# Optimization experiments

Measured on AMD Instinct MI355X. Metric: run time of the kernel, lower is better.

## Reference

```python
import jax, jax.numpy as jnp
import numpy as np

N_IN = 600000
KK = 4          # kernel_size**2 offsets for 2x2 transposed conv
C_IN = 64
C_OUT = 32
N_OUT = KK * N_IN
BN_EPS = 1e-5


def setup_inputs() -> dict:
    key = jax.random.key(0)
    k1, k2 = jax.random.split(key)
    x_feats = jax.random.normal(k1, (N_IN, C_IN), dtype=jnp.float32)
    # Kaiming-ish scale for conv weights [KK, C_IN, C_OUT]
    weight = jax.random.normal(k2, (KK, C_IN, C_OUT), dtype=jnp.float32) * (1.0 / np.sqrt(C_IN * KK))
    gamma = jnp.ones((C_OUT,), dtype=jnp.float32)
    beta = jnp.zeros((C_OUT,), dtype=jnp.float32)
    # Rulebook: with stride=2/kernel=2 each input voxel i has 4 child output
    # coords; out_spatial_sparsity stores outputs in arbitrary (hash) order, so
    # permute to get irregular scatter targets. out_idx[k, i] = output row for
    # (input i, kernel offset k).
    rng = np.random.default_rng(0)
    perm = rng.permutation(N_OUT).astype(np.int32)
    out_idx = jnp.asarray(perm.reshape(N_IN, KK).T)  # [KK, N_IN]
    return {
        "x_feats": x_feats,
        "weight": weight,
        "gamma": gamma,
        "beta": beta,
        "out_idx": out_idx,
        "n_out": N_OUT,
    }


def reference(x_feats, weight, gamma, beta, out_idx, n_out):
    # Gather-GEMM-scatter sparse transposed conv:
    # per-offset GEMM: [KK, N_IN, C_OUT]
    contrib = jnp.einsum("ni,kio->kno", x_feats, weight)
    y = jnp.zeros((n_out, contrib.shape[-1]), dtype=x_feats.dtype)
    y = y.at[out_idx.reshape(-1)].add(contrib.reshape(-1, contrib.shape[-1]))
    # BatchNorm1d (training mode: batch statistics, biased var) + ReLU
    mean = jnp.mean(y, axis=0)
    var = jnp.mean(jnp.square(y - mean), axis=0)
    y_hat = (y - mean) * jax.lax.rsqrt(var + BN_EPS) * gamma + beta
    return jax.nn.relu(y_hat)
```

## Files before the change

kernel.cpp:

```cpp
#include <hip/hip_runtime.h>

#define N_IN 600000
#define KK 4
#define C_IN 64
#define C_OUT 32
#define NTOT (KK*N_IN)
#define BN_EPS 1e-5f

typedef __attribute__((ext_vector_type(8))) short short8b;
typedef __attribute__((ext_vector_type(4))) float f32x4;

#define WS_G 0
#define WS_S 4096
#define WS_SCALE 4160
#define WS_BIAS 4192
#define WS_WFRAG 4224
#define WS_PART 8320
#define PART_STRIDE 4160

__device__ __forceinline__ unsigned short f2bf(float f) {
    unsigned int u = __float_as_uint(f);
    u += 0x7fffu + ((u >> 16) & 1u);
    return (unsigned short)(u >> 16);
}

union FragU { uint4 u; short8b s; unsigned int w[4]; };

#define GPADC 68
__global__ __launch_bounds__(256) void k_gram(const float* __restrict__ x,
                                              float* __restrict__ ws, int nblk) {
    __shared__ unsigned int sm[32 * GPADC];
    const int t = threadIdx.x, wv = t >> 6, l = t & 63;
    const int il = l & 15, g = l >> 4;
    const int chunk = t & 7, r0 = t >> 3;

    FragU ones;
    ones.u = make_uint4(0x3f803f80u, 0x3f803f80u, 0x3f803f80u, 0x3f803f80u);

    f32x4 acc[4];
    f32x4 accs = (f32x4){0.f, 0.f, 0.f, 0.f};
#pragma unroll
    for (int j = 0; j < 4; ++j) acc[j] = (f32x4){0.f, 0.f, 0.f, 0.f};

    const int ntiles = N_IN / 64;
    for (int tile = blockIdx.x; tile < ntiles; tile += nblk) {
        const float* base = x + (size_t)tile * 4096;
        const float4* pa = (const float4*)(base + (2 * r0) * 64 + chunk * 8);
        const float4* pb = (const float4*)(base + (2 * r0 + 1) * 64 + chunk * 8);
        const float4 a0 = pa[0], a1 = pa[1];
        const float4 b0 = pb[0], b1 = pb[1];
        __syncthreads();
        unsigned int pk[8];
        pk[0] = (unsigned)f2bf(a0.x) | ((unsigned)f2bf(b0.x) << 16);
        pk[1] = (unsigned)f2bf(a0.y) | ((unsigned)f2bf(b0.y) << 16);
        pk[2] = (unsigned)f2bf(a0.z) | ((unsigned)f2bf(b0.z) << 16);
        pk[3] = (unsigned)f2bf(a0.w) | ((unsigned)f2bf(b0.w) << 16);
        pk[4] = (unsigned)f2bf(a1.x) | ((unsigned)f2bf(b1.x) << 16);
        pk[5] = (unsigned)f2bf(a1.y) | ((unsigned)f2bf(b1.y) << 16);
        pk[6] = (unsigned)f2bf(a1.z) | ((unsigned)f2bf(b1.z) << 16);
        pk[7] = (unsigned)f2bf(a1.w) | ((unsigned)f2bf(b1.w) << 16);
        unsigned int* dst = sm + r0 * GPADC + chunk * 8;
        *(uint4*)dst = make_uint4(pk[0], pk[1], pk[2], pk[3]);
        *(uint4*)(dst + 4) = make_uint4(pk[4], pk[5], pk[6], pk[7]);
        __syncthreads();
#pragma unroll
        for (int s = 0; s < 2; ++s) {
            short8b fr[4];
#pragma unroll
            for (int c = 0; c < 4; ++c) {
                FragU fu;
#pragma unroll
                for (int h = 0; h < 4; ++h)
                    fu.w[h] = sm[(s * 16 + g * 4 + h) * GPADC + c * 16 + il];
                fr[c] = fu.s;
            }
#pragma unroll
            for (int tj = 0; tj < 4; ++tj)
                acc[tj] = __builtin_amdgcn_mfma_f32_16x16x32_bf16(fr[wv], fr[tj], acc[tj], 0, 0, 0);
            accs = __builtin_amdgcn_mfma_f32_16x16x32_bf16(ones.s, fr[wv], accs, 0, 0, 0);
        }
    }
    float* part = ws + WS_PART + (size_t)blockIdx.x * PART_STRIDE;
#pragma unroll
    for (int tj = 0; tj < 4; ++tj)
#pragma unroll
        for (int q = 0; q < 4; ++q)
            part[(wv * 16 + g * 4 + q) * 64 + tj * 16 + il] = acc[tj][q];
    if (g == 0) part[4096 + wv * 16 + il] = accs[0];
}

__global__ __launch_bounds__(256) void k_reduce(float* __restrict__ ws, int nba) {
    const int g = blockIdx.x * 4 + (threadIdx.x >> 6);
    const int lane = threadIdx.x & 63;
    const float* p = ws + WS_PART + g;
    float s = 0.f;
    for (int b = lane; b < nba; b += 64) s += p[(size_t)b * PART_STRIDE];
#pragma unroll
    for (int m = 1; m < 64; m <<= 1) s += __shfl_xor(s, m, 64);
    if (lane == 0) ws[g] = s;
}

__global__ __launch_bounds__(256) void k_finalize(const float* __restrict__ w,
                                                  const float* __restrict__ gamma,
                                                  const float* __restrict__ beta,
                                                  float* __restrict__ ws) {
    __shared__ float Gs[4096];
    __shared__ float ssum[64];
    __shared__ float red1[256], red2[256];
    const int t = threadIdx.x;
    for (int i = t; i < 4096; i += 256) Gs[i] = ws[i];
    if (t < 64) ssum[t] = ws[WS_S + t];
    __syncthreads();
    const int sub = t >> 7;
    const int k = (t >> 5) & 3;
    const int o = t & 31;
    float wc[64];
#pragma unroll
    for (int i = 0; i < 64; ++i) wc[i] = w[(k * 64 + i) * 32 + o];
    float m1 = 0.f, m2 = 0.f;
    for (int ii = 0; ii < 32; ++ii) {
        int i = sub * 32 + ii;
        m1 = fmaf(ssum[i], wc[i], m1);
        float ti = 0.f;
#pragma unroll
        for (int j = 0; j < 64; ++j) ti = fmaf(Gs[i * 64 + j], wc[j], ti);
        m2 = fmaf(wc[i], ti, m2);
    }
    red1[t] = m1;
    red2[t] = m2;
    __syncthreads();
    if (t < 32) {
        float s1 = 0.f, s2 = 0.f;
#pragma unroll
        for (int q = 0; q < 8; ++q) {
            int idx = (q & 3) * 32 + (q >> 2) * 128 + t;
            s1 += red1[idx];
            s2 += red2[idx];
        }
        float inv = 1.f / (float)NTOT;
        float mean = s1 * inv;
        float var = s2 * inv - mean * mean;
        float rstd = rsqrtf(var + BN_EPS);
        float sc = gamma[t] * rstd;
        ws[WS_SCALE + t] = sc;
        ws[WS_BIAS + t] = beta[t] - mean * sc;
    }
}

__global__ __launch_bounds__(256) void k_prepw(const float* __restrict__ w,
                                               float* __restrict__ ws) {
    const int t = blockIdx.x * 256 + threadIdx.x;
    const int l = t & 63;
    const int s = (t >> 6) & 1;
    const int c = t >> 7;
    const int col = c * 16 + (l & 15);
    const int kk = col >> 5, o = col & 31;
    unsigned int pk[4];
#pragma unroll
    for (int jj = 0; jj < 4; ++jj) {
        const int k0 = s * 32 + ((l >> 4) << 3) + jj * 2;
        unsigned int b0 = f2bf(w[(kk * 64 + k0) * 32 + o]);
        unsigned int b1 = f2bf(w[(kk * 64 + k0 + 1) * 32 + o]);
        pk[jj] = b0 | (b1 << 16);
    }
    uint4* dst = (uint4*)(ws + WS_WFRAG);
    dst[t] = make_uint4(pk[0], pk[1], pk[2], pk[3]);
}

__global__ __launch_bounds__(256, 3) void k_main(const float* __restrict__ x,
                                                 const int* __restrict__ oidx,
                                                 const float* __restrict__ ws,
                                                 float* __restrict__ out) {
    __shared__ float ldsD[4][64 * 32];
    __shared__ int ldsO[4][64];
    const int t = threadIdx.x, wv = t >> 6, l = t & 63;
    const int il = l & 15, g = l >> 4;
    const int c8 = l & 7, g8 = l >> 3;

    const float sc0 = ws[WS_SCALE + il], sc1 = ws[WS_SCALE + 16 + il];
    const float bs0 = ws[WS_BIAS + il], bs1 = ws[WS_BIAS + 16 + il];

    const short8b* wfs = (const short8b*)(ws + WS_WFRAG);
    short8b bwf[16];
#pragma unroll
    for (int f = 0; f < 16; ++f) bwf[f] = wfs[f * 64 + l];

    float* myD = ldsD[wv];
    int* myO = ldsO[wv];

    const int wgid = blockIdx.x * 4 + wv;
    int rowbase = wgid * 80;

    float4 cur0, cur1, cur2, cur3;
    {
        const float4* ap = (const float4*)(x + (size_t)(rowbase + il) * 64 + g * 8);
        cur0 = ap[0]; cur1 = ap[1]; cur2 = ap[8]; cur3 = ap[9];
    }
    int orow_cur = oidx[g * N_IN + rowbase + il];

#pragma unroll
    for (int it = 0; it < 5; ++it) {
        myO[l] = orow_cur;

        FragU af0, af1;
        af0.w[0] = (unsigned)f2bf(cur0.x) | ((unsigned)f2bf(cur0.y) << 16);
        af0.w[1] = (unsigned)f2bf(cur0.z) | ((unsigned)f2bf(cur0.w) << 16);
        af0.w[2] = (unsigned)f2bf(cur1.x) | ((unsigned)f2bf(cur1.y) << 16);
        af0.w[3] = (unsigned)f2bf(cur1.z) | ((unsigned)f2bf(cur1.w) << 16);
        af1.w[0] = (unsigned)f2bf(cur2.x) | ((unsigned)f2bf(cur2.y) << 16);
        af1.w[1] = (unsigned)f2bf(cur2.z) | ((unsigned)f2bf(cur2.w) << 16);
        af1.w[2] = (unsigned)f2bf(cur3.x) | ((unsigned)f2bf(cur3.y) << 16);
        af1.w[3] = (unsigned)f2bf(cur3.z) | ((unsigned)f2bf(cur3.w) << 16);

        float4 nx0{}, nx1{}, nx2{}, nx3{};
        int orow_nxt = 0;
        if (it < 4) {
            const float4* ap = (const float4*)(x + (size_t)(rowbase + 16 + il) * 64 + g * 8);
            nx0 = ap[0]; nx1 = ap[1]; nx2 = ap[8]; nx3 = ap[9];
            orow_nxt = oidx[g * N_IN + rowbase + 16 + il];
        }

        f32x4 acc[8];
#pragma unroll
        for (int c = 0; c < 8; ++c) acc[c] = (f32x4){0.f, 0.f, 0.f, 0.f};
#pragma unroll
        for (int c = 0; c < 8; ++c)
            acc[c] = __builtin_amdgcn_mfma_f32_16x16x32_bf16(af0.s, bwf[c * 2 + 0], acc[c], 0, 0, 0);
#pragma unroll
        for (int c = 0; c < 8; ++c)
            acc[c] = __builtin_amdgcn_mfma_f32_16x16x32_bf16(af1.s, bwf[c * 2 + 1], acc[c], 0, 0, 0);

#pragma unroll
        for (int c = 0; c < 8; ++c) {
            const float sc = (c & 1) ? sc1 : sc0;
            const float bs = (c & 1) ? bs1 : bs0;
            const int ch = (c & 1) * 16 + il;
            const int cc = ch >> 2, wd = ch & 3;
            const int rb = (c >> 1) * 16 + g * 4;
#pragma unroll
            for (int q = 0; q < 4; ++q) {
                const int R = rb + q;
                const float v = fmaxf(0.f, fmaf(acc[c][q], sc, bs));
                myD[R * 32 + (((cc ^ (R & 7)) << 2) | wd)] = v;
            }
        }
#pragma unroll
        for (int m = 0; m < 8; ++m) {
            const int R = m * 8 + g8;
            const float4 v = *(const float4*)(myD + R * 32 + ((c8 ^ g8) << 2));
            const int orow = myO[R];
            *(float4*)(out + (size_t)orow * 32 + c8 * 4) = v;
        }

        rowbase += 16;
        cur0 = nx0; cur1 = nx1; cur2 = nx2; cur3 = nx3;
        orow_cur = orow_nxt;
    }
}

extern "C" void kernel_launch(void* const* d_in, const int* in_sizes, int n_in,
                              void* d_out, int out_size, void* d_ws, size_t ws_size,
                              hipStream_t stream) {
    const float* x = (const float*)d_in[0];
    const float* w = (const float*)d_in[1];
    const float* gamma = (const float*)d_in[2];
    const float* beta = (const float*)d_in[3];
    const int* oidx = (const int*)d_in[4];
    float* out = (float*)d_out;
    float* ws = (float*)d_ws;

    int nba = 1024;
    size_t cap = ws_size / sizeof(float);
    if (cap < (size_t)WS_PART + (size_t)nba * PART_STRIDE) {
        size_t fit = (cap - WS_PART) / PART_STRIDE;
        nba = (int)(fit < 1 ? 1 : fit);
        if (nba > 1024) nba = 1024;
    }

    hipLaunchKernelGGL(k_prepw, dim3(4), dim3(256), 0, stream, w, ws);
    hipLaunchKernelGGL(k_gram, dim3(nba), dim3(256), 0, stream, x, ws, nba);
    hipLaunchKernelGGL(k_reduce, dim3(1040), dim3(256), 0, stream, ws, nba);
    hipLaunchKernelGGL(k_finalize, dim3(1), dim3(256), 0, stream, w, gamma, beta, ws);
    hipLaunchKernelGGL(k_main, dim3(1875), dim3(256), 0, stream, x, oidx, ws, out);
}
```

Before: 231.5 us.

## Invert scatter rulebook to gather inputs and write outputs contiguously

Adds a kernel that builds the inverse of the output index map in workspace, then rewrites the main kernel to walk output rows in order. Each row gathers its source input row, runs the full 4-offset GEMM, selects the matching offset's result and writes coalesced output. This swaps random 128-byte output scatters for random input-row gathers plus an extra inverse-map scatter pass. It also computes 4x redundant MFMA work per row and drops the workspace-size fallback.

```diff
diff --git a/kernel.cpp b/kernel.cpp
--- a/kernel.cpp
+++ b/kernel.cpp
@@ -17,6 +17,8 @@
 #define WS_WFRAG 4224
 #define WS_PART 8320
 #define PART_STRIDE 4160
+#define NBA_MAX 1024
+#define WS_INV (WS_PART + NBA_MAX * PART_STRIDE)
 
 __device__ __forceinline__ unsigned short f2bf(float f) {
     unsigned int u = __float_as_uint(f);
@@ -25,6 +27,12 @@
 }
 
 union FragU { uint4 u; short8b s; unsigned int w[4]; };
+
+__global__ __launch_bounds__(256) void k_binv(const int* __restrict__ oidx,
+                                              int* __restrict__ inv) {
+    const int j = blockIdx.x * 256 + threadIdx.x;
+    if (j < NTOT) inv[oidx[j]] = j;
+}
 
 #define GPADC 68
 __global__ __launch_bounds__(256) void k_gram(const float* __restrict__ x,
@@ -167,15 +175,13 @@
     dst[t] = make_uint4(pk[0], pk[1], pk[2], pk[3]);
 }
 
-__global__ __launch_bounds__(256, 3) void k_main(const float* __restrict__ x,
-                                                 const int* __restrict__ oidx,
+__global__ __launch_bounds__(256, 3) void k_minv(const float* __restrict__ x,
+                                                 const int* __restrict__ inv,
                                                  const float* __restrict__ ws,
                                                  float* __restrict__ out) {
-    __shared__ float ldsD[4][64 * 32];
-    __shared__ int ldsO[4][64];
+    __shared__ float ldsT[4][16 * 32];
     const int t = threadIdx.x, wv = t >> 6, l = t & 63;
     const int il = l & 15, g = l >> 4;
-    const int c8 = l & 7, g8 = l >> 3;
 
     const float sc0 = ws[WS_SCALE + il], sc1 = ws[WS_SCALE + 16 + il];
     const float bs0 = ws[WS_BIAS + il], bs1 = ws[WS_BIAS + 16 + il];
@@ -185,22 +191,32 @@
 #pragma unroll
     for (int f = 0; f < 16; ++f) bwf[f] = wfs[f * 64 + l];
 
-    float* myD = ldsD[wv];
-    int* myO = ldsO[wv];
-
+    float* myT = ldsT[wv];
     const int wgid = blockIdx.x * 4 + wv;
-    int rowbase = wgid * 80;
-
+    const int base0 = wgid * 240;
+
+    int j0 = inv[base0 + il];
+    int k_cur = (j0 >= N_IN) + (j0 >= 2 * N_IN) + (j0 >= 3 * N_IN);
+    int i_cur = j0 - k_cur * N_IN;
     float4 cur0, cur1, cur2, cur3;
     {
-        const float4* ap = (const float4*)(x + (size_t)(rowbase + il) * 64 + g * 8);
+        const float4* ap = (const float4*)(x + (size_t)i_cur * 64 + g * 8);
         cur0 = ap[0]; cur1 = ap[1]; cur2 = ap[8]; cur3 = ap[9];
     }
-    int orow_cur = oidx[g * N_IN + rowbase + il];
-
-#pragma unroll
-    for (int it = 0; it < 5; ++it) {
-        myO[l] = orow_cur;
+    int j1 = inv[base0 + 16 + il];
+
+#pragma unroll 1
+    for (int it = 0; it < 15; ++it) {
+        const int base = base0 + it * 16;
+        int j2 = j1;
+        if (it < 13) j2 = inv[base + 32 + il];
+        int k_nxt = (j1 >= N_IN) + (j1 >= 2 * N_IN) + (j1 >= 3 * N_IN);
+        int i_nxt = j1 - k_nxt * N_IN;
+        float4 nx0 = cur0, nx1 = cur1, nx2 = cur2, nx3 = cur3;
+        if (it < 14) {
+            const float4* ap = (const float4*)(x + (size_t)i_nxt * 64 + g * 8);
+            nx0 = ap[0]; nx1 = ap[1]; nx2 = ap[8]; nx3 = ap[9];
+        }
 
         FragU af0, af1;
         af0.w[0] = (unsigned)f2bf(cur0.x) | ((unsigned)f2bf(cur0.y) << 16);
@@ -212,14 +228,6 @@
         af1.w[2] = (unsigned)f2bf(cur3.x) | ((unsigned)f2bf(cur3.y) << 16);
         af1.w[3] = (unsigned)f2bf(cur3.z) | ((unsigned)f2bf(cur3.w) << 16);
 
-        float4 nx0{}, nx1{}, nx2{}, nx3{};
-        int orow_nxt = 0;
-        if (it < 4) {
-            const float4* ap = (const float4*)(x + (size_t)(rowbase + 16 + il) * 64 + g * 8);
-            nx0 = ap[0]; nx1 = ap[1]; nx2 = ap[8]; nx3 = ap[9];
-            orow_nxt = oidx[g * N_IN + rowbase + 16 + il];
-        }
-
         f32x4 acc[8];
 #pragma unroll
         for (int c = 0; c < 8; ++c) acc[c] = (f32x4){0.f, 0.f, 0.f, 0.f};
@@ -231,30 +239,32 @@
             acc[c] = __builtin_amdgcn_mfma_f32_16x16x32_bf16(af1.s, bwf[c * 2 + 1], acc[c], 0, 0, 0);
 
 #pragma unroll
-        for (int c = 0; c < 8; ++c) {
-            const float sc = (c & 1) ? sc1 : sc0;
-            const float bs = (c & 1) ? bs1 : bs0;
-            const int ch = (c & 1) * 16 + il;
-            const int cc = ch >> 2, wd = ch & 3;
-            const int rb = (c >> 1) * 16 + g * 4;
-#pragma unroll
-            for (int q = 0; q < 4; ++q) {
-                const int R = rb + q;
-                const float v = fmaxf(0.f, fmaf(acc[c][q], sc, bs));
-                myD[R * 32 + (((cc ^ (R & 7)) << 2) | wd)] = v;
-            }
-        }
-#pragma unroll
-        for (int m = 0; m < 8; ++m) {
-            const int R = m * 8 + g8;
-            const float4 v = *(const float4*)(myD + R * 32 + ((c8 ^ g8) << 2));
-            const int orow = myO[R];
-            *(float4*)(out + (size_t)orow * 32 + c8 * 4) = v;
-        }
-
-        rowbase += 16;
+        for (int q = 0; q < 4; ++q) {
+            const int r = g * 4 + q;
+            const int kq = __shfl(k_cur, r, 64);
+            const float lo = (kq == 0) ? acc[0][q] : (kq == 1) ? acc[2][q] : (kq == 2) ? acc[4][q] : acc[6][q];
+            const float hi = (kq == 0) ? acc[1][q] : (kq == 1) ? acc[3][q] : (kq == 2) ? acc[5][q] : acc[7][q];
+            const float vlo = fmaxf(0.f, fmaf(lo, sc0, bs0));
+            const float vhi = fmaxf(0.f, fmaf(hi, sc1, bs1));
+            const int ccl = il >> 2, wd = il & 3, rx = r & 7;
+            myT[r * 32 + (((ccl ^ rx) << 2) | wd)] = vlo;
+            myT[r * 32 + ((((ccl + 4) ^ rx) << 2) | wd)] = vhi;
+        }
+        {
+            const int r = l >> 2;
+            const int cbase = (l & 3) * 2;
+            const int cpc0 = (cbase + 0) ^ (r & 7);
+            const int cpc1 = (cbase + 1) ^ (r & 7);
+            const float4 v0 = *(const float4*)(myT + r * 32 + (cpc0 << 2));
+            const float4 v1 = *(const float4*)(myT + r * 32 + (cpc1 << 2));
+            float* op = out + (size_t)base * 32 + l * 8;
+            *(float4*)op = v0;
+            *(float4*)(op + 4) = v1;
+        }
+
         cur0 = nx0; cur1 = nx1; cur2 = nx2; cur3 = nx3;
-        orow_cur = orow_nxt;
+        k_cur = k_nxt;
+        j1 = j2;
     }
 }
 
@@ -268,18 +278,14 @@
     const int* oidx = (const int*)d_in[4];
     float* out = (float*)d_out;
     float* ws = (float*)d_ws;
-
-    int nba = 1024;
-    size_t cap = ws_size / sizeof(float);
-    if (cap < (size_t)WS_PART + (size_t)nba * PART_STRIDE) {
-        size_t fit = (cap - WS_PART) / PART_STRIDE;
-        nba = (int)(fit < 1 ? 1 : fit);
-        if (nba > 1024) nba = 1024;
-    }
+    int* inv = (int*)(ws + WS_INV);
+
+    int nba = NBA_MAX;
 
     hipLaunchKernelGGL(k_prepw, dim3(4), dim3(256), 0, stream, w, ws);
+    hipLaunchKernelGGL(k_binv, dim3((NTOT + 255) / 256), dim3(256), 0, stream, oidx, inv);
     hipLaunchKernelGGL(k_gram, dim3(nba), dim3(256), 0, stream, x, ws, nba);
     hipLaunchKernelGGL(k_reduce, dim3(1040), dim3(256), 0, stream, ws, nba);
     hipLaunchKernelGGL(k_finalize, dim3(1), dim3(256), 0, stream, w, gamma, beta, ws);
-    hipLaunchKernelGGL(k_main, dim3(1875), dim3(256), 0, stream, x, oidx, ws, out);
-}
+    hipLaunchKernelGGL(k_minv, dim3(2500), dim3(256), 0, stream, x, inv, ws, out);
+}
```

New measurement: 327.0 us. 41.2% more time.
